# Optimization experiments

Hardware: AMD Instinct MI355X
Metric: run time of the kernel (lower is better)

## Reference

```python
import jax, jax.numpy as jnp
import numpy as np

N_NODES = 50000
N_EDGES = 800000
NFEAT = 512
NHID = 64
NHEADS = 8
NCLASS = 40
ALPHA = 0.2  # LeakyReLU slope
EPS = 1e-16  # guards isolated-node division


def setup_inputs() -> dict:
    key = jax.random.key(0)
    k = jax.random.split(key, 6)
    x = jax.random.normal(k[0], (N_NODES, NFEAT), dtype=jnp.float32)
    W_heads = jax.random.normal(k[1], (NHEADS, NFEAT, NHID), dtype=jnp.float32) * 0.05
    a_heads = jax.random.normal(k[2], (NHEADS, 2 * NHID), dtype=jnp.float32) * 0.05
    W_out = jax.random.normal(k[3], (NHEADS * NHID, NCLASS), dtype=jnp.float32) * 0.05
    a_out = jax.random.normal(k[4], (2 * NCLASS,), dtype=jnp.float32) * 0.05
    edge_index = jax.random.randint(k[5], (2, N_EDGES), 0, N_NODES, dtype=jnp.int32)
    return {"x": x, "W_heads": W_heads, "a_heads": a_heads,
            "W_out": W_out, "a_out": a_out, "edge_index": edge_index}


def _gat_layer(x, W, a, row, col, concat):
    # pyGAT sparse layer: h = xW; e_ij = exp(-LeakyReLU(a^T [h_i || h_j]));
    # out_i = sum_j e_ij h_j / sum_j e_ij   (aggregate into row, gather from col)
    D = W.shape[1]
    h = x @ W                                            # [N, D]
    score = h[row] @ a[:D] + h[col] @ a[D:]              # [E]
    e = jnp.exp(-jax.nn.leaky_relu(score, ALPHA))        # [E]
    num = jax.ops.segment_sum(e[:, None] * h[col], row, num_segments=x.shape[0])  # [N, D]
    den = jax.ops.segment_sum(e, row, num_segments=x.shape[0])                    # [N]
    out = num / (den[:, None] + EPS)
    return jax.nn.elu(out) if concat else out


def reference(x, W_heads, a_heads, W_out, a_out, edge_index):
    # dropout layers are identity in eval mode (training=False)
    row, col = edge_index[0], edge_index[1]
    heads = jax.vmap(lambda W, a: _gat_layer(x, W, a, row, col, True))(W_heads, a_heads)
    # [H, N, D] -> [N, H*D] (concat along feature dim, head-major like torch.cat)
    hcat = jnp.transpose(heads, (1, 0, 2)).reshape(x.shape[0], -1)
    return _gat_layer(hcat, W_out, a_out, row, col, False)  # [N, NCLASS]
```

## Files before the change

### kernel.cpp

```cpp
#include <hip/hip_runtime.h>
#include <hip/hip_bf16.h>

#define N_NODES 50000
#define N_EDGES 800000
#define NFEAT   512
#define NHID    64
#define NHEADS  8
#define NCLASS  40
#define HD      (NHEADS*NHID)
#define ALPHA   0.2f
#define EPS_F   1e-16f
#define NCHUNK  ((N_NODES + 255)/256)

typedef __attribute__((ext_vector_type(8))) short short8;
typedef __attribute__((ext_vector_type(4))) float floatx4;

__device__ __forceinline__ float bf2f(unsigned short u) {
    union { unsigned int i; float f; } v; v.i = ((unsigned int)u) << 16; return v.f;
}
__device__ __forceinline__ unsigned short f2bf(float f) {
    union { __hip_bfloat16 h; unsigned short u; } cv;
    cv.h = __float2bfloat16(f);
    return cv.u;
}

__global__ void repackWb(const float* __restrict__ Wh, unsigned short* __restrict__ Wrb) {
    int idx = blockIdx.x*256 + threadIdx.x;
    if (idx >= 512*512) return;
    int n = idx >> 9, k = idx & 511;
    int hd = n >> 6, d = n & 63;
    Wrb[idx] = f2bf(Wh[(size_t)hd*NFEAT*NHID + (size_t)k*NHID + d]);
}

__global__ void repackWout(const float* __restrict__ Wo, unsigned short* __restrict__ Wob) {
    int idx = blockIdx.x*256 + threadIdx.x;
    if (idx >= 64*512) return;
    int n = idx >> 9, k = idx & 511;
    float v = (n < NCLASS) ? Wo[(size_t)k*NCLASS + n] : 0.f;
    Wob[idx] = f2bf(v);
}

__global__ __launch_bounds__(256) void mfma_gemm1(const float* __restrict__ A,
                                                  const unsigned short* __restrict__ Bbf,
                                                  unsigned short* __restrict__ H1p, int M) {
    __shared__ short Asl[128*40];
    __shared__ short Bsl[128*40];
    int tid  = threadIdx.x;
    int wid  = tid >> 6, lane = tid & 63;
    int lrow = lane & 15, quad = lane >> 4;
    int wm = wid & 1, wn = wid >> 1;
    int row0 = blockIdx.y * 128, col0 = blockIdx.x * 128;

    floatx4 acc[4][4];
#pragma unroll
    for (int mm = 0; mm < 4; mm++)
#pragma unroll
        for (int nn = 0; nn < 4; nn++) acc[mm][nn] = (floatx4){0.f,0.f,0.f,0.f};

    for (int k0 = 0; k0 < 512; k0 += 32) {
#pragma unroll
        for (int it = 0; it < 2; ++it) {
            int q  = tid + it*256;
            int r  = q >> 2, kk = (q & 3) * 8;
            int ar = row0 + r; ar = ar < M ? ar : M - 1;
            const float* src = A + (size_t)ar*512 + k0 + kk;
            float4 f0 = *(const float4*)src;
            float4 f1 = *(const float4*)(src + 4);
            short8 h;
            h[0] = (short)f2bf(f0.x); h[1] = (short)f2bf(f0.y);
            h[2] = (short)f2bf(f0.z); h[3] = (short)f2bf(f0.w);
            h[4] = (short)f2bf(f1.x); h[5] = (short)f2bf(f1.y);
            h[6] = (short)f2bf(f1.z); h[7] = (short)f2bf(f1.w);
            *(short8*)(&Asl[r*40 + kk]) = h;
            *(short8*)(&Bsl[r*40 + kk]) =
                *(const short8*)(Bbf + (size_t)(col0 + r)*512 + k0 + kk);
        }
        __syncthreads();
        short8 af[4], bfr[4];
#pragma unroll
        for (int mm = 0; mm < 4; ++mm)
            af[mm] = *(const short8*)(&Asl[(wm*64 + mm*16 + lrow)*40 + quad*8]);
#pragma unroll
        for (int nn = 0; nn < 4; ++nn)
            bfr[nn] = *(const short8*)(&Bsl[(wn*64 + nn*16 + lrow)*40 + quad*8]);
#pragma unroll
        for (int mm = 0; mm < 4; ++mm)
#pragma unroll
            for (int nn = 0; nn < 4; ++nn)
                acc[mm][nn] = __builtin_amdgcn_mfma_f32_16x16x32_bf16(
                    af[mm], bfr[nn], acc[mm][nn], 0, 0, 0);
        __syncthreads();
    }

#pragma unroll
    for (int mm = 0; mm < 4; ++mm) {
        int rbase = row0 + wm*64 + mm*16 + quad*4;
#pragma unroll
        for (int nn = 0; nn < 4; ++nn) {
            int c = col0 + wn*64 + nn*16 + lrow;
            int off = (c & 63)*8 + (c >> 6);
#pragma unroll
            for (int r = 0; r < 4; ++r) {
                int grow = rbase + r;
                if (grow < M)
                    H1p[(size_t)grow*512 + off] = f2bf(acc[mm][nn][r]);
            }
        }
    }
}

__global__ __launch_bounds__(256) void mfma_gemm2(const unsigned short* __restrict__ Abf,
                                                  const unsigned short* __restrict__ Bbf,
                                                  float* __restrict__ H2, int M) {
    __shared__ short Asl[256*40];
    __shared__ short Bsl[64*40];
    int tid  = threadIdx.x;
    int wid  = tid >> 6, lane = tid & 63;
    int lrow = lane & 15, quad = lane >> 4;
    int row0 = blockIdx.x * 256;

    floatx4 acc[4][4];
#pragma unroll
    for (int mm = 0; mm < 4; mm++)
#pragma unroll
        for (int nn = 0; nn < 4; nn++) acc[mm][nn] = (floatx4){0.f,0.f,0.f,0.f};

    for (int k0 = 0; k0 < 512; k0 += 32) {
#pragma unroll
        for (int it = 0; it < 4; ++it) {
            int q  = tid + it*256;
            int r  = q >> 2, kk = (q & 3) * 8;
            int ar = row0 + r; ar = ar < M ? ar : M - 1;
            *(short8*)(&Asl[r*40 + kk]) =
                *(const short8*)(Abf + (size_t)ar*512 + k0 + kk);
        }
        {
            int r = tid >> 2, kk = (tid & 3) * 8;
            *(short8*)(&Bsl[r*40 + kk]) =
                *(const short8*)(Bbf + (size_t)r*512 + k0 + kk);
        }
        __syncthreads();
        short8 af[4], bfr[4];
#pragma unroll
        for (int mm = 0; mm < 4; ++mm)
            af[mm] = *(const short8*)(&Asl[(wid*64 + mm*16 + lrow)*40 + quad*8]);
#pragma unroll
        for (int nn = 0; nn < 4; ++nn)
            bfr[nn] = *(const short8*)(&Bsl[(nn*16 + lrow)*40 + quad*8]);
#pragma unroll
        for (int mm = 0; mm < 4; ++mm)
#pragma unroll
            for (int nn = 0; nn < 4; ++nn)
                acc[mm][nn] = __builtin_amdgcn_mfma_f32_16x16x32_bf16(
                    af[mm], bfr[nn], acc[mm][nn], 0, 0, 0);
        __syncthreads();
    }

#pragma unroll
    for (int mm = 0; mm < 4; ++mm) {
        int rbase = row0 + wid*64 + mm*16 + quad*4;
#pragma unroll
        for (int nn = 0; nn < 4; ++nn) {
            int c = nn*16 + lrow;
            if (c < NCLASS) {
#pragma unroll
                for (int r = 0; r < 4; ++r) {
                    int grow = rbase + r;
                    if (grow < M)
                        H2[(size_t)grow*NCLASS + c] = acc[mm][nn][r];
                }
            }
        }
    }
}

__global__ __launch_bounds__(256) void dots1(const unsigned short* __restrict__ H1p,
                                             const float* __restrict__ a_heads,
                                             float* __restrict__ srcdot,
                                             float* __restrict__ dstdot) {
    int wave = (blockIdx.x*256 + threadIdx.x) >> 6;
    int lane = threadIdx.x & 63;
    if (wave >= N_NODES) return;
    short8 hv = *(const short8*)(H1p + (size_t)wave*512 + lane*8);
    float s0[8], s1[8];
#pragma unroll
    for (int j = 0; j < 8; j++) {
        float h = bf2f((unsigned short)hv[j]);
        s0[j] = h * a_heads[j*128 + lane];
        s1[j] = h * a_heads[j*128 + 64 + lane];
    }
#pragma unroll
    for (int off = 32; off > 0; off >>= 1) {
#pragma unroll
        for (int j = 0; j < 8; j++) {
            s0[j] += __shfl_down(s0[j], off, 64);
            s1[j] += __shfl_down(s1[j], off, 64);
        }
    }
    if (lane == 0) {
#pragma unroll
        for (int j = 0; j < 8; j++) {
            srcdot[wave*8 + j] = s0[j];
            dstdot[wave*8 + j] = s1[j];
        }
    }
}

__global__ void zero_deg(int* __restrict__ deg) {
    int i = blockIdx.x*256 + threadIdx.x;
    if (i < N_NODES) deg[i] = 0;
}
__global__ void histk(const int* __restrict__ row, int* __restrict__ deg) {
    int e = blockIdx.x*256 + threadIdx.x;
    if (e < N_EDGES) atomicAdd(&deg[row[e]], 1);
}
__global__ void scanA(const int* __restrict__ deg, int* __restrict__ row_ptr,
                      int* __restrict__ chunk_tot) {
    __shared__ int s[256];
    int t = threadIdx.x;
    int idx = blockIdx.x*256 + t;
    int v = (idx < N_NODES) ? deg[idx] : 0;
    s[t] = v;
    __syncthreads();
#pragma unroll
    for (int off = 1; off < 256; off <<= 1) {
        int x = (t >= off) ? s[t-off] : 0;
        __syncthreads();
        s[t] += x;
        __syncthreads();
    }
    if (idx < N_NODES) row_ptr[idx] = s[t] - v;
    if (t == 255) chunk_tot[blockIdx.x] = s[t];
}
__global__ void scanB(const int* __restrict__ chunk_tot, int* __restrict__ chunk_off,
                      int* __restrict__ row_ptr) {
    __shared__ int s[256];
    int t = threadIdx.x;
    int v = (t < NCHUNK) ? chunk_tot[t] : 0;
    s[t] = v;
    __syncthreads();
#pragma unroll
    for (int off = 1; off < 256; off <<= 1) {
        int x = (t >= off) ? s[t-off] : 0;
        __syncthreads();
        s[t] += x;
        __syncthreads();
    }
    if (t < NCHUNK) chunk_off[t] = s[t] - v;
    if (t == 255) row_ptr[N_NODES] = s[t];
}
__global__ void scanC(const int* __restrict__ chunk_off, int* __restrict__ row_ptr,
                      int* __restrict__ cursor) {
    int idx = blockIdx.x*256 + threadIdx.x;
    if (idx < N_NODES) {
        int rp = row_ptr[idx] + chunk_off[idx >> 8];
        row_ptr[idx] = rp;
        cursor[idx] = rp;
    }
}

__global__ void fillk_w1(const int* __restrict__ row, const int* __restrict__ col,
                         const float* __restrict__ srcdot, const float* __restrict__ dstdot,
                         int* __restrict__ cursor, int* __restrict__ csr_col,
                         int* __restrict__ pose, float* __restrict__ Wcsr) {
    int e = blockIdx.x*256 + threadIdx.x;
    if (e >= N_EDGES) return;
    int r = row[e], c = col[e];
    int pos = atomicAdd(&cursor[r], 1);
    csr_col[pos] = c;
    pose[e] = pos;
    float4 sa = *(const float4*)(srcdot + (size_t)r*8);
    float4 sb = *(const float4*)(srcdot + (size_t)r*8 + 4);
    float4 da = *(const float4*)(dstdot + (size_t)c*8);
    float4 db = *(const float4*)(dstdot + (size_t)c*8 + 4);
    float s[8] = {sa.x+da.x, sa.y+da.y, sa.z+da.z, sa.w+da.w,
                  sb.x+db.x, sb.y+db.y, sb.z+db.z, sb.w+db.w};
    float o[8];
#pragma unroll
    for (int j = 0; j < 8; j++) {
        float lr = s[j] > 0.f ? s[j] : ALPHA*s[j];
        o[j] = __expf(-lr);
    }
    *(float4*)(Wcsr + (size_t)pos*8)     = make_float4(o[0], o[1], o[2], o[3]);
    *(float4*)(Wcsr + (size_t)pos*8 + 4) = make_float4(o[4], o[5], o[6], o[7]);
}

__global__ __launch_bounds__(256) void agg1(const unsigned short* __restrict__ H1p,
                                            const float* __restrict__ Wcsr,
                                            const int* __restrict__ row_ptr,
                                            const int* __restrict__ csr_col,
                                            unsigned short* __restrict__ hcatb) {
    int wave = (blockIdx.x*256 + threadIdx.x) >> 6;
    int lane = threadIdx.x & 63;
    if (wave >= N_NODES) return;
    int start = row_ptr[wave], end = row_ptr[wave+1];
    float acc[8], den[8];
#pragma unroll
    for (int j = 0; j < 8; j++) { acc[j] = 0.f; den[j] = 0.f; }

    int k = start;
    for (; k + 2 <= end; k += 2) {
        int c0 = csr_col[k], c1 = csr_col[k+1];
        float4 wa0 = *(const float4*)(Wcsr + (size_t)k*8);
        float4 wb0 = *(const float4*)(Wcsr + (size_t)k*8 + 4);
        float4 wa1 = *(const float4*)(Wcsr + (size_t)k*8 + 8);
        float4 wb1 = *(const float4*)(Wcsr + (size_t)k*8 + 12);
        short8 hv0 = *(const short8*)(H1p + (size_t)c0*512 + lane*8);
        short8 hv1 = *(const short8*)(H1p + (size_t)c1*512 + lane*8);
        float w0[8] = {wa0.x, wa0.y, wa0.z, wa0.w, wb0.x, wb0.y, wb0.z, wb0.w};
        float w1[8] = {wa1.x, wa1.y, wa1.z, wa1.w, wb1.x, wb1.y, wb1.z, wb1.w};
#pragma unroll
        for (int j = 0; j < 8; j++) {
            den[j] += w0[j] + w1[j];
            acc[j] = fmaf(w0[j], bf2f((unsigned short)hv0[j]), acc[j]);
            acc[j] = fmaf(w1[j], bf2f((unsigned short)hv1[j]), acc[j]);
        }
    }
    for (; k < end; ++k) {
        int c = csr_col[k];
        float4 wa = *(const float4*)(Wcsr + (size_t)k*8);
        float4 wb = *(const float4*)(Wcsr + (size_t)k*8 + 4);
        short8 hv = *(const short8*)(H1p + (size_t)c*512 + lane*8);
        float w[8] = {wa.x, wa.y, wa.z, wa.w, wb.x, wb.y, wb.z, wb.w};
#pragma unroll
        for (int j = 0; j < 8; j++) {
            den[j] += w[j];
            acc[j] = fmaf(w[j], bf2f((unsigned short)hv[j]), acc[j]);
        }
    }
#pragma unroll
    for (int j = 0; j < 8; j++) {
        float o = acc[j] / (den[j] + EPS_F);
        o = o > 0.f ? o : (__expf(o) - 1.f);
        hcatb[(size_t)wave*HD + j*64 + lane] = f2bf(o);
    }
}

__global__ void dots2(const float* __restrict__ H2, const float* __restrict__ a_out,
                      float* __restrict__ src2, float* __restrict__ dst2) {
    int i = blockIdx.x*256 + threadIdx.x;
    if (i >= N_NODES) return;
    float s0 = 0.f, s1 = 0.f;
#pragma unroll
    for (int c = 0; c < NCLASS; c++) {
        float h = H2[(size_t)i*NCLASS + c];
        s0 = fmaf(h, a_out[c], s0);
        s1 = fmaf(h, a_out[NCLASS + c], s1);
    }
    src2[i] = s0; dst2[i] = s1;
}

__global__ void edge_w2(const int* __restrict__ row, const int* __restrict__ col,
                        const int* __restrict__ pose,
                        const float* __restrict__ src2, const float* __restrict__ dst2,
                        float* __restrict__ w2csr) {
    int e = blockIdx.x*256 + threadIdx.x;
    if (e >= N_EDGES) return;
    float s = src2[row[e]] + dst2[col[e]];
    float lr = s > 0.f ? s : ALPHA*s;
    w2csr[pose[e]] = __expf(-lr);
}

__global__ __launch_bounds__(256) void agg2(const float* __restrict__ H2,
                                            const float* __restrict__ w2csr,
                                            const int* __restrict__ row_ptr,
                                            const int* __restrict__ csr_col,
                                            float* __restrict__ out) {
    int wave = (blockIdx.x*256 + threadIdx.x) >> 6;
    int lane = threadIdx.x & 63;
    if (wave >= N_NODES) return;
    int start = row_ptr[wave], end = row_ptr[wave+1];
    int l = lane < NCLASS ? lane : 0;
    float acc = 0.f, den = 0.f;
    int k = start;
    for (; k + 4 <= end; k += 4) {
        float4 wv = *(const float4*)(w2csr + k);
        int c0 = csr_col[k],   c1 = csr_col[k+1], c2 = csr_col[k+2], c3 = csr_col[k+3];
        float h0 = H2[(size_t)c0*NCLASS + l];
        float h1 = H2[(size_t)c1*NCLASS + l];
        float h2 = H2[(size_t)c2*NCLASS + l];
        float h3 = H2[(size_t)c3*NCLASS + l];
        den += (wv.x + wv.y) + (wv.z + wv.w);
        acc = fmaf(wv.x, h0, acc);
        acc = fmaf(wv.y, h1, acc);
        acc = fmaf(wv.z, h2, acc);
        acc = fmaf(wv.w, h3, acc);
    }
    for (; k < end; ++k) {
        int c = csr_col[k];
        float w = w2csr[k];
        den += w;
        acc = fmaf(w, H2[(size_t)c*NCLASS + l], acc);
    }
    if (lane < NCLASS)
        out[(size_t)wave*NCLASS + lane] = acc / (den + EPS_F);
}

extern "C" void kernel_launch(void* const* d_in, const int* in_sizes, int n_in,
                              void* d_out, int out_size, void* d_ws, size_t ws_size,
                              hipStream_t stream) {
    const float* x       = (const float*)d_in[0];
    const float* W_heads = (const float*)d_in[1];
    const float* a_heads = (const float*)d_in[2];
    const float* W_out   = (const float*)d_in[3];
    const float* a_out   = (const float*)d_in[4];
    const int*   ei      = (const int*)d_in[5];
    const int*   row     = ei;
    const int*   col     = ei + N_EDGES;
    float* out = (float*)d_out;

    char* ws = (char*)d_ws;
    size_t off = 0;
    auto alloc = [&](size_t bytes) {
        char* p = ws + off;
        off = (off + bytes + 255) & ~(size_t)255;
        return p;
    };
    unsigned short* Wrb   = (unsigned short*)alloc((size_t)512*512*2);
    unsigned short* Wob   = (unsigned short*)alloc((size_t)64*512*2);
    unsigned short* H1p   = (unsigned short*)alloc((size_t)N_NODES*HD*2);
    unsigned short* hcatb = (unsigned short*)alloc((size_t)N_NODES*HD*2);
    float* srcdot  = (float*)alloc((size_t)N_NODES*NHEADS*4);
    float* dstdot  = (float*)alloc((size_t)N_NODES*NHEADS*4);
    float* Wcsr    = (float*)alloc((size_t)N_EDGES*NHEADS*4);
    int*   deg     = (int*)alloc((size_t)N_NODES*4);
    int*   row_ptr = (int*)alloc((size_t)(N_NODES+1)*4);
    int*   cursor  = (int*)alloc((size_t)N_NODES*4);
    int*   ctot    = (int*)alloc(256*4);
    int*   coff    = (int*)alloc(256*4);
    int*   csr_col = (int*)alloc((size_t)N_EDGES*4);
    int*   pose    = (int*)alloc((size_t)N_EDGES*4);
    float* H2      = (float*)alloc((size_t)N_NODES*NCLASS*4);
    float* src2    = (float*)alloc((size_t)N_NODES*4);
    float* dst2    = (float*)alloc((size_t)N_NODES*4);
    float* w2csr   = (float*)alloc((size_t)N_EDGES*4);
    (void)ws_size;

    const int EB = (N_EDGES + 255)/256;
    const int NB = (N_NODES + 255)/256;
    const int WB = (N_NODES*64 + 255)/256;

    repackWb<<<(512*512 + 255)/256, 256, 0, stream>>>(W_heads, Wrb);
    repackWout<<<(64*512 + 255)/256, 256, 0, stream>>>(W_out, Wob);
    {
        dim3 grid(4, (N_NODES + 127)/128);
        mfma_gemm1<<<grid, 256, 0, stream>>>(x, Wrb, H1p, N_NODES);
    }
    dots1<<<WB, 256, 0, stream>>>(H1p, a_heads, srcdot, dstdot);

    zero_deg<<<NB, 256, 0, stream>>>(deg);
    histk<<<EB, 256, 0, stream>>>(row, deg);
    scanA<<<NCHUNK, 256, 0, stream>>>(deg, row_ptr, ctot);
    scanB<<<1, 256, 0, stream>>>(ctot, coff, row_ptr);
    scanC<<<NCHUNK, 256, 0, stream>>>(coff, row_ptr, cursor);
    fillk_w1<<<EB, 256, 0, stream>>>(row, col, srcdot, dstdot, cursor,
                                     csr_col, pose, Wcsr);

    agg1<<<WB, 256, 0, stream>>>(H1p, Wcsr, row_ptr, csr_col, hcatb);

    mfma_gemm2<<<(N_NODES + 255)/256, 256, 0, stream>>>(hcatb, Wob, H2, N_NODES);
    dots2<<<NB, 256, 0, stream>>>(H2, a_out, src2, dst2);
    edge_w2<<<EB, 256, 0, stream>>>(row, col, pose, src2, dst2, w2csr);
    agg2<<<WB, 256, 0, stream>>>(H2, w2csr, row_ptr, csr_col, out);
}
```

Before: 578.7 us.

## Widen gemm1 to full-N tiles, fuse layer-2 edge weights into agg2, trim kernels

gemm1 now uses 512-thread blocks that each cover all 512 output columns for a 128-row tile, so x is read and converted to bf16 only once instead of four times. The second-layer edge-weight kernel and its pose/w2csr buffers are removed, and agg2 computes the LeakyReLU/exp weights on the fly from src2/dst2. H2 is padded to 64 columns for aligned gathers, agg1 is unrolled to 4 edges per iteration, and the degree zeroing is folded into repackWb. In exchange, gemm1 needs more LDS and registers per block, and agg2 does extra random dst2 gathers and exp work per edge.

```diff
diff --git a/kernel.cpp b/kernel.cpp
--- a/kernel.cpp
+++ b/kernel.cpp
@@ -24,8 +24,10 @@
     return cv.u;
 }
 
-__global__ void repackWb(const float* __restrict__ Wh, unsigned short* __restrict__ Wrb) {
+__global__ void repackWb(const float* __restrict__ Wh, unsigned short* __restrict__ Wrb,
+                         int* __restrict__ deg) {
     int idx = blockIdx.x*256 + threadIdx.x;
+    if (idx < N_NODES) deg[idx] = 0;
     if (idx >= 512*512) return;
     int n = idx >> 9, k = idx & 511;
     int hd = n >> 6, d = n & 63;
@@ -40,28 +42,27 @@
     Wob[idx] = f2bf(v);
 }
 
-__global__ __launch_bounds__(256) void mfma_gemm1(const float* __restrict__ A,
-                                                  const unsigned short* __restrict__ Bbf,
-                                                  unsigned short* __restrict__ H1p, int M) {
+__global__ __launch_bounds__(512, 2) void mfma_gemm1(const float* __restrict__ A,
+                                                     const unsigned short* __restrict__ Bbf,
+                                                     unsigned short* __restrict__ H1p, int M) {
     __shared__ short Asl[128*40];
-    __shared__ short Bsl[128*40];
+    __shared__ short Bsl[512*40];
     int tid  = threadIdx.x;
     int wid  = tid >> 6, lane = tid & 63;
     int lrow = lane & 15, quad = lane >> 4;
     int wm = wid & 1, wn = wid >> 1;
-    int row0 = blockIdx.y * 128, col0 = blockIdx.x * 128;
-
-    floatx4 acc[4][4];
+    int row0 = blockIdx.x * 128;
+    if (row0 >= M) return;
+
+    floatx4 acc[4][8];
 #pragma unroll
     for (int mm = 0; mm < 4; mm++)
 #pragma unroll
-        for (int nn = 0; nn < 4; nn++) acc[mm][nn] = (floatx4){0.f,0.f,0.f,0.f};
+        for (int nn = 0; nn < 8; nn++) acc[mm][nn] = (floatx4){0.f,0.f,0.f,0.f};
 
     for (int k0 = 0; k0 < 512; k0 += 32) {
-#pragma unroll
-        for (int it = 0; it < 2; ++it) {
-            int q  = tid + it*256;
-            int r  = q >> 2, kk = (q & 3) * 8;
+        {
+            int r = tid >> 2, kk = (tid & 3) * 8;
             int ar = row0 + r; ar = ar < M ? ar : M - 1;
             const float* src = A + (size_t)ar*512 + k0 + kk;
             float4 f0 = *(const float4*)src;
@@ -72,21 +73,26 @@
             h[4] = (short)f2bf(f1.x); h[5] = (short)f2bf(f1.y);
             h[6] = (short)f2bf(f1.z); h[7] = (short)f2bf(f1.w);
             *(short8*)(&Asl[r*40 + kk]) = h;
+        }
+#pragma unroll
+        for (int it = 0; it < 4; ++it) {
+            int q = tid + it*512;
+            int r = q >> 2, kk = (q & 3) * 8;
             *(short8*)(&Bsl[r*40 + kk]) =
-                *(const short8*)(Bbf + (size_t)(col0 + r)*512 + k0 + kk);
-        }
-        __syncthreads();
-        short8 af[4], bfr[4];
+                *(const short8*)(Bbf + (size_t)r*512 + k0 + kk);
+        }
+        __syncthreads();
+        short8 af[4], bfr[8];
 #pragma unroll
         for (int mm = 0; mm < 4; ++mm)
             af[mm] = *(const short8*)(&Asl[(wm*64 + mm*16 + lrow)*40 + quad*8]);
 #pragma unroll
-        for (int nn = 0; nn < 4; ++nn)
-            bfr[nn] = *(const short8*)(&Bsl[(wn*64 + nn*16 + lrow)*40 + quad*8]);
+        for (int nn = 0; nn < 8; ++nn)
+            bfr[nn] = *(const short8*)(&Bsl[(wn*128 + nn*16 + lrow)*40 + quad*8]);
 #pragma unroll
         for (int mm = 0; mm < 4; ++mm)
 #pragma unroll
-            for (int nn = 0; nn < 4; ++nn)
+            for (int nn = 0; nn < 8; ++nn)
                 acc[mm][nn] = __builtin_amdgcn_mfma_f32_16x16x32_bf16(
                     af[mm], bfr[nn], acc[mm][nn], 0, 0, 0);
         __syncthreads();
@@ -96,8 +102,8 @@
     for (int mm = 0; mm < 4; ++mm) {
         int rbase = row0 + wm*64 + mm*16 + quad*4;
 #pragma unroll
-        for (int nn = 0; nn < 4; ++nn) {
-            int c = col0 + wn*64 + nn*16 + lrow;
+        for (int nn = 0; nn < 8; ++nn) {
+            int c = wn*128 + nn*16 + lrow;
             int off = (c & 63)*8 + (c >> 6);
 #pragma unroll
             for (int r = 0; r < 4; ++r) {
@@ -111,7 +117,7 @@
 
 __global__ __launch_bounds__(256) void mfma_gemm2(const unsigned short* __restrict__ Abf,
                                                   const unsigned short* __restrict__ Bbf,
-                                                  float* __restrict__ H2, int M) {
+                                                  float* __restrict__ H2p, int M) {
     __shared__ short Asl[256*40];
     __shared__ short Bsl[64*40];
     int tid  = threadIdx.x;
@@ -162,13 +168,11 @@
 #pragma unroll
         for (int nn = 0; nn < 4; ++nn) {
             int c = nn*16 + lrow;
-            if (c < NCLASS) {
-#pragma unroll
-                for (int r = 0; r < 4; ++r) {
-                    int grow = rbase + r;
-                    if (grow < M)
-                        H2[(size_t)grow*NCLASS + c] = acc[mm][nn][r];
-                }
+#pragma unroll
+            for (int r = 0; r < 4; ++r) {
+                int grow = rbase + r;
+                if (grow < M)
+                    H2p[(size_t)grow*64 + c] = acc[mm][nn][r];
             }
         }
     }
@@ -206,10 +210,6 @@
     }
 }
 
-__global__ void zero_deg(int* __restrict__ deg) {
-    int i = blockIdx.x*256 + threadIdx.x;
-    if (i < N_NODES) deg[i] = 0;
-}
 __global__ void histk(const int* __restrict__ row, int* __restrict__ deg) {
     int e = blockIdx.x*256 + threadIdx.x;
     if (e < N_EDGES) atomicAdd(&deg[row[e]], 1);
@@ -262,13 +262,12 @@
 __global__ void fillk_w1(const int* __restrict__ row, const int* __restrict__ col,
                          const float* __restrict__ srcdot, const float* __restrict__ dstdot,
                          int* __restrict__ cursor, int* __restrict__ csr_col,
-                         int* __restrict__ pose, float* __restrict__ Wcsr) {
+                         float* __restrict__ Wcsr) {
     int e = blockIdx.x*256 + threadIdx.x;
     if (e >= N_EDGES) return;
     int r = row[e], c = col[e];
     int pos = atomicAdd(&cursor[r], 1);
     csr_col[pos] = c;
-    pose[e] = pos;
     float4 sa = *(const float4*)(srcdot + (size_t)r*8);
     float4 sb = *(const float4*)(srcdot + (size_t)r*8 + 4);
     float4 da = *(const float4*)(dstdot + (size_t)c*8);
@@ -299,21 +298,28 @@
     for (int j = 0; j < 8; j++) { acc[j] = 0.f; den[j] = 0.f; }
 
     int k = start;
-    for (; k + 2 <= end; k += 2) {
-        int c0 = csr_col[k], c1 = csr_col[k+1];
-        float4 wa0 = *(const float4*)(Wcsr + (size_t)k*8);
-        float4 wb0 = *(const float4*)(Wcsr + (size_t)k*8 + 4);
-        float4 wa1 = *(const float4*)(Wcsr + (size_t)k*8 + 8);
-        float4 wb1 = *(const float4*)(Wcsr + (size_t)k*8 + 12);
+    for (; k + 4 <= end; k += 4) {
+        int c0 = csr_col[k],   c1 = csr_col[k+1];
+        int c2 = csr_col[k+2], c3 = csr_col[k+3];
         short8 hv0 = *(const short8*)(H1p + (size_t)c0*512 + lane*8);
         short8 hv1 = *(const short8*)(H1p + (size_t)c1*512 + lane*8);
-        float w0[8] = {wa0.x, wa0.y, wa0.z, wa0.w, wb0.x, wb0.y, wb0.z, wb0.w};
-        float w1[8] = {wa1.x, wa1.y, wa1.z, wa1.w, wb1.x, wb1.y, wb1.z, wb1.w};
+        short8 hv2 = *(const short8*)(H1p + (size_t)c2*512 + lane*8);
+        short8 hv3 = *(const short8*)(H1p + (size_t)c3*512 + lane*8);
+        float4 wv[8];
+#pragma unroll
+        for (int q = 0; q < 8; q++)
+            wv[q] = *(const float4*)(Wcsr + (size_t)k*8 + q*4);
+        const float* w0 = (const float*)&wv[0];
+        const float* w1 = (const float*)&wv[2];
+        const float* w2 = (const float*)&wv[4];
+        const float* w3 = (const float*)&wv[6];
 #pragma unroll
         for (int j = 0; j < 8; j++) {
-            den[j] += w0[j] + w1[j];
+            den[j] += (w0[j] + w1[j]) + (w2[j] + w3[j]);
             acc[j] = fmaf(w0[j], bf2f((unsigned short)hv0[j]), acc[j]);
             acc[j] = fmaf(w1[j], bf2f((unsigned short)hv1[j]), acc[j]);
+            acc[j] = fmaf(w2[j], bf2f((unsigned short)hv2[j]), acc[j]);
+            acc[j] = fmaf(w3[j], bf2f((unsigned short)hv3[j]), acc[j]);
         }
     }
     for (; k < end; ++k) {
@@ -336,33 +342,23 @@
     }
 }
 
-__global__ void dots2(const float* __restrict__ H2, const float* __restrict__ a_out,
+__global__ void dots2(const float* __restrict__ H2p, const float* __restrict__ a_out,
                       float* __restrict__ src2, float* __restrict__ dst2) {
     int i = blockIdx.x*256 + threadIdx.x;
     if (i >= N_NODES) return;
     float s0 = 0.f, s1 = 0.f;
 #pragma unroll
     for (int c = 0; c < NCLASS; c++) {
-        float h = H2[(size_t)i*NCLASS + c];
+        float h = H2p[(size_t)i*64 + c];
         s0 = fmaf(h, a_out[c], s0);
         s1 = fmaf(h, a_out[NCLASS + c], s1);
     }
     src2[i] = s0; dst2[i] = s1;
 }
 
-__global__ void edge_w2(const int* __restrict__ row, const int* __restrict__ col,
-                        const int* __restrict__ pose,
-                        const float* __restrict__ src2, const float* __restrict__ dst2,
-                        float* __restrict__ w2csr) {
-    int e = blockIdx.x*256 + threadIdx.x;
-    if (e >= N_EDGES) return;
-    float s = src2[row[e]] + dst2[col[e]];
-    float lr = s > 0.f ? s : ALPHA*s;
-    w2csr[pose[e]] = __expf(-lr);
-}
-
-__global__ __launch_bounds__(256) void agg2(const float* __restrict__ H2,
-                                            const float* __restrict__ w2csr,
+__global__ __launch_bounds__(256) void agg2(const float* __restrict__ H2p,
+                                            const float* __restrict__ src2,
+                                            const float* __restrict__ dst2,
                                             const int* __restrict__ row_ptr,
                                             const int* __restrict__ csr_col,
                                             float* __restrict__ out) {
@@ -370,27 +366,36 @@
     int lane = threadIdx.x & 63;
     if (wave >= N_NODES) return;
     int start = row_ptr[wave], end = row_ptr[wave+1];
+    float s2i = src2[wave];
     int l = lane < NCLASS ? lane : 0;
     float acc = 0.f, den = 0.f;
     int k = start;
     for (; k + 4 <= end; k += 4) {
-        float4 wv = *(const float4*)(w2csr + k);
-        int c0 = csr_col[k],   c1 = csr_col[k+1], c2 = csr_col[k+2], c3 = csr_col[k+3];
-        float h0 = H2[(size_t)c0*NCLASS + l];
-        float h1 = H2[(size_t)c1*NCLASS + l];
-        float h2 = H2[(size_t)c2*NCLASS + l];
-        float h3 = H2[(size_t)c3*NCLASS + l];
-        den += (wv.x + wv.y) + (wv.z + wv.w);
-        acc = fmaf(wv.x, h0, acc);
-        acc = fmaf(wv.y, h1, acc);
-        acc = fmaf(wv.z, h2, acc);
-        acc = fmaf(wv.w, h3, acc);
+        int c0 = csr_col[k],   c1 = csr_col[k+1];
+        int c2 = csr_col[k+2], c3 = csr_col[k+3];
+        float t0 = s2i + dst2[c0], t1 = s2i + dst2[c1];
+        float t2 = s2i + dst2[c2], t3 = s2i + dst2[c3];
+        float h0 = H2p[(size_t)c0*64 + l];
+        float h1 = H2p[(size_t)c1*64 + l];
+        float h2 = H2p[(size_t)c2*64 + l];
+        float h3 = H2p[(size_t)c3*64 + l];
+        t0 = t0 > 0.f ? t0 : ALPHA*t0;  float w0 = __expf(-t0);
+        t1 = t1 > 0.f ? t1 : ALPHA*t1;  float w1 = __expf(-t1);
+        t2 = t2 > 0.f ? t2 : ALPHA*t2;  float w2 = __expf(-t2);
+        t3 = t3 > 0.f ? t3 : ALPHA*t3;  float w3 = __expf(-t3);
+        den += (w0 + w1) + (w2 + w3);
+        acc = fmaf(w0, h0, acc);
+        acc = fmaf(w1, h1, acc);
+        acc = fmaf(w2, h2, acc);
+        acc = fmaf(w3, h3, acc);
     }
     for (; k < end; ++k) {
         int c = csr_col[k];
-        float w = w2csr[k];
+        float t = s2i + dst2[c];
+        t = t > 0.f ? t : ALPHA*t;
+        float w = __expf(-t);
         den += w;
-        acc = fmaf(w, H2[(size_t)c*NCLASS + l], acc);
+        acc = fmaf(w, H2p[(size_t)c*64 + l], acc);
     }
     if (lane < NCLASS)
         out[(size_t)wave*NCLASS + lane] = acc / (den + EPS_F);
@@ -429,37 +434,30 @@
     int*   ctot    = (int*)alloc(256*4);
     int*   coff    = (int*)alloc(256*4);
     int*   csr_col = (int*)alloc((size_t)N_EDGES*4);
-    int*   pose    = (int*)alloc((size_t)N_EDGES*4);
-    float* H2      = (float*)alloc((size_t)N_NODES*NCLASS*4);
+    float* H2p     = (float*)alloc((size_t)N_NODES*64*4);
     float* src2    = (float*)alloc((size_t)N_NODES*4);
     float* dst2    = (float*)alloc((size_t)N_NODES*4);
-    float* w2csr   = (float*)alloc((size_t)N_EDGES*4);
     (void)ws_size;
 
     const int EB = (N_EDGES + 255)/256;
+    const int WB = (N_NODES*64 + 255)/256;
     const int NB = (N_NODES + 255)/256;
-    const int WB = (N_NODES*64 + 255)/256;
-
-    repackWb<<<(512*512 + 255)/256, 256, 0, stream>>>(W_heads, Wrb);
+
+    repackWb<<<(512*512 + 255)/256, 256, 0, stream>>>(W_heads, Wrb, deg);
     repackWout<<<(64*512 + 255)/256, 256, 0, stream>>>(W_out, Wob);
-    {
-        dim3 grid(4, (N_NODES + 127)/128);
-        mfma_gemm1<<<grid, 256, 0, stream>>>(x, Wrb, H1p, N_NODES);
-    }
+    mfma_gemm1<<<(N_NODES + 127)/128, 512, 0, stream>>>(x, Wrb, H1p, N_NODES);
     dots1<<<WB, 256, 0, stream>>>(H1p, a_heads, srcdot, dstdot);
 
-    zero_deg<<<NB, 256, 0, stream>>>(deg);
     histk<<<EB, 256, 0, stream>>>(row, deg);
     scanA<<<NCHUNK, 256, 0, stream>>>(deg, row_ptr, ctot);
     scanB<<<1, 256, 0, stream>>>(ctot, coff, row_ptr);
     scanC<<<NCHUNK, 256, 0, stream>>>(coff, row_ptr, cursor);
     fillk_w1<<<EB, 256, 0, stream>>>(row, col, srcdot, dstdot, cursor,
-                                     csr_col, pose, Wcsr);
+                                     csr_col, Wcsr);
 
     agg1<<<WB, 256, 0, stream>>>(H1p, Wcsr, row_ptr, csr_col, hcatb);
 
-    mfma_gemm2<<<(N_NODES + 255)/256, 256, 0, stream>>>(hcatb, Wob, H2, N_NODES);
-    dots2<<<NB, 256, 0, stream>>>(H2, a_out, src2, dst2);
-    edge_w2<<<EB, 256, 0, stream>>>(row, col, pose, src2, dst2, w2csr);
-    agg2<<<WB, 256, 0, stream>>>(H2, w2csr, row_ptr, csr_col, out);
-}
+    mfma_gemm2<<<(N_NODES + 255)/256, 256, 0, stream>>>(hcatb, Wob, H2p, N_NODES);
+    dots2<<<NB, 256, 0, stream>>>(H2p, a_out, src2, dst2);
+    agg2<<<WB, 256, 0, stream>>>(H2p, src2, dst2, row_ptr, csr_col, out);
+}
```

Result: faster. 561.7 us (-2.9%).
